# Kernel tuning notes

Hardware: AMD Instinct MI355X
Metric: run time of the kernel (lower is better)

The kernel has to match this reference:

```python
import jax, jax.numpy as jnp
import numpy as np

N = 65536          # particles
E = 524288         # relations (avg degree 8)
RIG = 4096         # rigid instance = particles [0, RIG); fluid = [RIG, N)
PSTEPS = 2
ATTR, STATE, RELD, NF = 3, 6, 1, 128
DT = 1.0 / 60.0
MEAN_P = np.zeros(3, np.float32); STD_P = np.ones(3, np.float32)
MEAN_V = np.zeros(3, np.float32); STD_V = np.ones(3, np.float32)


def _lin(x, w, b):
    return x @ w.T + b  # torch Linear convention: w is [out, in]


def setup_inputs() -> dict:
    key = jax.random.key(0)
    ks = iter(jax.random.split(key, 40))
    d = {}
    d["state"] = jax.random.normal(next(ks), (N, STATE), jnp.float32)
    d["attr"] = jax.random.normal(next(ks), (N, ATTR), jnp.float32)
    d["Ra"] = jax.random.normal(next(ks), (E, RELD), jnp.float32)
    d["rel_recv"] = jax.random.randint(next(ks), (E,), 0, N, jnp.int32)
    d["rel_send"] = jax.random.randint(next(ks), (E,), 0, N, jnp.int32)

    def w(shape):
        return jax.random.normal(next(ks), shape, jnp.float32) / np.sqrt(shape[1])

    d["pe_w0"] = w((NF, ATTR + 2 * STATE)); d["pe_b0"] = jnp.zeros(NF)
    d["pe_w1"] = w((NF, NF)); d["pe_b1"] = jnp.zeros(NF)
    d["re_w0"] = w((NF, 2 * ATTR + 4 * STATE + RELD)); d["re_b0"] = jnp.zeros(NF)
    d["re_w1"] = w((NF, NF)); d["re_b1"] = jnp.zeros(NF)
    d["re_w2"] = w((NF, NF)); d["re_b2"] = jnp.zeros(NF)
    d["rp_w"] = w((NF, 3 * NF)); d["rp_b"] = jnp.zeros(NF)
    d["pp_w"] = w((NF, 2 * NF)); d["pp_b"] = jnp.zeros(NF)
    d["rg_w0"] = w((NF, NF)); d["rg_b0"] = jnp.zeros(NF)
    d["rg_w1"] = w((NF, NF)); d["rg_b1"] = jnp.zeros(NF)
    d["rg_w2"] = w((7, NF)); d["rg_b2"] = jnp.zeros(7)
    d["fl_w0"] = w((NF, NF)); d["fl_b0"] = jnp.zeros(NF)
    d["fl_w1"] = w((NF, NF)); d["fl_b1"] = jnp.zeros(NF)
    d["fl_w2"] = w((3, NF)); d["fl_b2"] = jnp.zeros(3)
    return d


def reference(state, attr, Ra, rel_recv, rel_send,
              pe_w0, pe_b0, pe_w1, pe_b1,
              re_w0, re_b0, re_w1, re_b1, re_w2, re_b2,
              rp_w, rp_b, pp_w, pp_b,
              rg_w0, rg_b0, rg_w1, rg_b1, rg_w2, rg_b2,
              fl_w0, fl_b0, fl_w1, fl_b1, fl_w2, fl_b2):
    relu = jax.nn.relu
    mean_p = jnp.asarray(MEAN_P); std_p = jnp.asarray(STD_P)
    mean_v = jnp.asarray(MEAN_V); std_v = jnp.asarray(STD_V)

    # rigid-body offset (state minus instance centroid for the rigid instance)
    offset = jnp.zeros_like(state).at[:RIG].set(
        state[:RIG] - jnp.mean(state[:RIG], axis=0))
    attr2 = jnp.concatenate([attr, offset], axis=1)        # [N, ATTR+STATE]

    # f_O^enc: particle encoder on [attr2, state]
    pe_in = jnp.concatenate([attr2, state], axis=1)         # [N, 15]
    particle_encode = relu(_lin(relu(_lin(pe_in, pe_w0, pe_b0)), pe_w1, pe_b1))

    # f_R^enc: relation encoder on gathered receiver/sender features
    rel_in = jnp.concatenate([attr2[rel_recv], attr2[rel_send],
                              state[rel_recv], state[rel_send], Ra], axis=1)  # [E, 31]
    h = relu(_lin(rel_in, re_w0, re_b0))
    h = relu(_lin(h, re_w1, re_b1))
    relation_encode = relu(_lin(h, re_w2, re_b2))           # [E, NF]

    # propagation: gather effects -> f_R -> scatter-add -> f_O
    effect = jnp.zeros((N, NF), state.dtype)
    for _ in range(PSTEPS):
        r_eff = effect[rel_recv]                            # [E, NF]
        s_eff = effect[rel_send]                            # [E, NF]
        rel_eff = relu(_lin(jnp.concatenate(
            [relation_encode, r_eff, s_eff], axis=1), rp_w, rp_b))
        agg = jax.ops.segment_sum(rel_eff, rel_recv, num_segments=N)  # Rr @ rel_eff
        effect = relu(_lin(jnp.concatenate(
            [particle_encode, agg], axis=1), pp_w, pp_b))   # residual=False

    # rigid predictor: quaternion + translation of the rigid body
    pooled = jnp.mean(effect[:RIG], axis=0)                 # [NF]
    t = _lin(relu(_lin(relu(_lin(pooled, rg_w0, rg_b0)), rg_w1, rg_b1)), rg_w2, rg_b2)
    q = t[:4] / jnp.linalg.norm(t[:4])
    w, x, y, z = q[0], q[1], q[2], q[3]
    R = jnp.stack([
        jnp.stack([1.0 - 2 * (y * y + z * z), 2 * (x * y + z * w), 2 * (x * z - y * w)]),
        jnp.stack([2 * (x * y - z * w), 1.0 - 2 * (x * x + z * z), 2 * (y * z + x * w)]),
        jnp.stack([2 * (x * z + y * w), 2 * (y * z - x * w), 1.0 - 2 * (x * x + y * y)]),
    ])
    b = t[4:] * std_p
    p0 = state[:RIG, :3] * std_p + mean_p
    c = jnp.mean(p0, axis=0)
    p1 = (p0 - c) @ R + b + c
    v = (p1 - p0) / DT
    pred_rigid = (v - mean_v) / std_v                       # [RIG, 3]

    # fluid predictor: per-particle MLP
    f = relu(_lin(effect[RIG:], fl_w0, fl_b0))
    f = relu(_lin(f, fl_w1, fl_b1))
    pred_fluid = _lin(f, fl_w2, fl_b2)                      # [N-RIG, 3]

    return jnp.concatenate([pred_rigid, pred_fluid], axis=0)  # [N, 3]
```

## Files before the change

kernel.cpp:

```cpp
#include <hip/hip_runtime.h>
#include <hip/hip_bf16.h>
#include <cstdio>

#define N_P   65536
#define N_E   524288
#define RIG_  4096

typedef __attribute__((ext_vector_type(8))) short bf16x8;
typedef __attribute__((ext_vector_type(4))) float f32x4;
typedef unsigned short u16;
typedef unsigned int   u32;

__device__ __forceinline__ u16 f2b(float x) {
    __hip_bfloat16 h = __float2bfloat16(x);
    return *(u16*)&h;
}
__device__ __forceinline__ float b2f(u16 u) {
    union { unsigned u; float f; } c; c.u = ((unsigned)u) << 16; return c.f;
}
__device__ __forceinline__ unsigned pk2(float x, float y) {
    return (unsigned)f2b(x) | ((unsigned)f2b(y) << 16);
}
#define MFMA(a,b,c) __builtin_amdgcn_mfma_f32_16x16x32_bf16((a),(b),(c),0,0,0)

__global__ __launch_bounds__(256) void k_hist(const int* __restrict__ recv,
                                              u32* __restrict__ cnt) {
    int i = blockIdx.x * 256 + threadIdx.x;
    if (i < N_E) atomicAdd(&cnt[recv[i]], 1u);
}
__global__ __launch_bounds__(256) void k_scan1(u32* __restrict__ data,
                                               u32* __restrict__ bsum) {
    __shared__ u32 s[256];
    int t = threadIdx.x, g = blockIdx.x * 256 + t;
    u32 v = data[g];
    s[t] = v; __syncthreads();
    for (int o = 1; o < 256; o <<= 1) {
        u32 x = (t >= o) ? s[t - o] : 0u;
        __syncthreads(); s[t] += x; __syncthreads();
    }
    data[g] = s[t] - v;
    if (t == 255) bsum[blockIdx.x] = s[255];
}
__global__ __launch_bounds__(256) void k_scan2(u32* __restrict__ bsum) {
    __shared__ u32 s[256];
    int t = threadIdx.x;
    u32 v = bsum[t];
    s[t] = v; __syncthreads();
    for (int o = 1; o < 256; o <<= 1) {
        u32 x = (t >= o) ? s[t - o] : 0u;
        __syncthreads(); s[t] += x; __syncthreads();
    }
    bsum[t] = s[t] - v;
}
__global__ __launch_bounds__(256) void k_scan3(u32* __restrict__ data,
                                               const u32* __restrict__ bsum) {
    int g = blockIdx.x * 256 + threadIdx.x;
    data[g] += bsum[blockIdx.x];
}
__global__ __launch_bounds__(256) void k_scatter(const int* __restrict__ recv,
                                                 const int* __restrict__ send,
                                                 u32* __restrict__ head,
                                                 u32* __restrict__ perm,
                                                 int* __restrict__ srecv,
                                                 int* __restrict__ ssend) {
    int i = blockIdx.x * 256 + threadIdx.x;
    if (i < N_E) {
        int n = recv[i];
        u32 pos = atomicAdd(&head[n], 1u);
        perm[pos] = (u32)i;
        srecv[pos] = n;
        ssend[pos] = send[i];
    }
}

struct CvtJob { const float* src; u16* dst; int n; int mode; int bstart; };
struct CvtArgs { CvtJob j[14]; };

__global__ __launch_bounds__(256) void k_cvt_all(CvtArgs a) {
    int b = blockIdx.x;
    int ji = 0;
    #pragma unroll
    for (int k = 1; k < 14; k++) if (b >= a.j[k].bstart) ji = k;
    CvtJob jb = a.j[ji];
    int i = (b - jb.bstart) * 256 + threadIdx.x;
    if (i >= jb.n) return;
    if (jb.mode == 0) {
        jb.dst[i] = f2b(jb.src[i]);
    } else if (jb.mode == 2) {
        int r = i >> 7;
        jb.dst[i] = (r < 3) ? f2b(jb.src[i]) : 0;
    } else if (jb.mode == 3) {
        int r = i >> 7, c = i & 127;
        jb.dst[i] = f2b(jb.src[r * 384 + c]);
    } else if (jb.mode == 4) {
        int r = i >> 7, c = i & 127;
        jb.dst[i] = f2b(jb.src[r * 256 + c]);
    } else if (jb.mode == 5) {
        int r = i >> 5, c = i & 31;
        float v = 0.f;
        if (c < 9)       v = jb.src[r * 31 + c];
        else if (c < 15) v = jb.src[r * 31 + 18 + (c - 9)];
        jb.dst[i] = f2b(v);
    } else if (jb.mode == 6) {
        int r = i >> 5, c = i & 31;
        float v = 0.f;
        if (c < 9)       v = jb.src[r * 31 + 9 + c];
        else if (c < 15) v = jb.src[r * 31 + 24 + (c - 9)];
        jb.dst[i] = f2b(v);
    } else {
        int r = i >> 5, c = i & 31;
        jb.dst[i] = (c < 15) ? f2b(jb.src[r * 15 + c]) : 0;
    }
}

__global__ __launch_bounds__(256) void k_centroid(const float* __restrict__ state,
                                                  float* __restrict__ cent) {
    int d = blockIdx.x;
    __shared__ float red[256];
    float s = 0.f;
    for (int r = threadIdx.x; r < RIG_; r += 256) s += state[r * 6 + d];
    red[threadIdx.x] = s; __syncthreads();
    for (int o = 128; o > 0; o >>= 1) {
        if (threadIdx.x < o) red[threadIdx.x] += red[threadIdx.x + o];
        __syncthreads();
    }
    if (threadIdx.x == 0) cent[d] = red[0] / (float)RIG_;
}

__global__ __launch_bounds__(256) void k_particle_ext(
        const float* __restrict__ state, const float* __restrict__ attr,
        const float* __restrict__ cent,
        const u16* __restrict__ w0r, const u16* __restrict__ w0s,
        const u16* __restrict__ pew0, const float* __restrict__ pe_b0,
        const u16* __restrict__ pew1, const float* __restrict__ pe_b1,
        const u16* __restrict__ wp,
        u16* __restrict__ P, u16* __restrict__ Q, u16* __restrict__ T) {
    __shared__ float in_s[64][16];
    __shared__ u16 INF[64 * 32];
    __shared__ __align__(16) u16 BUF[64 * 128];
    __shared__ float b0_s[128], b1_s[128];
    int t = threadIdx.x;
    int base = blockIdx.x * 64;
    if (t < 128) { b0_s[t] = pe_b0[t]; b1_s[t] = pe_b1[t]; }
    for (int it = t; it < 64 * 15; it += 256) {
        int r = it / 15, c = it % 15;
        int p = base + r;
        float v;
        if (c < 3)      v = attr[p * 3 + c];
        else if (c < 9) v = (p < RIG_) ? (state[p * 6 + (c - 3)] - cent[c - 3]) : 0.0f;
        else            v = state[p * 6 + (c - 9)];
        in_s[r][c] = v;
    }
    __syncthreads();
    int wv = t >> 6, kq4 = (t >> 4) & 3, m = t & 15;
    {
        int e = wv * 16 + m;
        u16 tmp[8];
        #pragma unroll
        for (int j = 0; j < 8; j++) {
            int k = kq4 * 8 + j;
            tmp[j] = (k < 15) ? f2b(in_s[e][k]) : (u16)0;
        }
        *(uint4*)&INF[((wv * 4 + kq4) * 16 + m) * 8] = *(uint4*)tmp;
    }
    int lane = t & 63, mm = lane & 15, quad = lane >> 4;
    bf16x8 af0 = *(const bf16x8*)&INF[((wv * 4 + quad) * 16 + mm) * 8];
    {
        f32x4 acc[8] = {};
        #pragma unroll
        for (int nt = 0; nt < 8; nt++) {
            bf16x8 bf = *(const bf16x8*)(w0r + (size_t)(nt * 16 + mm) * 32 + quad * 8);
            acc[nt] = MFMA(af0, bf, acc[nt]);
        }
        #pragma unroll
        for (int nt = 0; nt < 8; nt++) {
            int col = nt * 16 + mm;
            #pragma unroll
            for (int rg = 0; rg < 4; rg++) {
                int row = wv * 16 + quad * 4 + rg;
                P[(size_t)(base + row) * 128 + col] = f2b(acc[nt][rg]);
            }
        }
    }
    {
        f32x4 acc[8] = {};
        #pragma unroll
        for (int nt = 0; nt < 8; nt++) {
            bf16x8 bf = *(const bf16x8*)(w0s + (size_t)(nt * 16 + mm) * 32 + quad * 8);
            acc[nt] = MFMA(af0, bf, acc[nt]);
        }
        #pragma unroll
        for (int nt = 0; nt < 8; nt++) {
            int col = nt * 16 + mm;
            #pragma unroll
            for (int rg = 0; rg < 4; rg++) {
                int row = wv * 16 + quad * 4 + rg;
                Q[(size_t)(base + row) * 128 + col] = f2b(acc[nt][rg]);
            }
        }
    }
    {
        f32x4 acc[8] = {};
        #pragma unroll
        for (int nt = 0; nt < 8; nt++) {
            bf16x8 bf = *(const bf16x8*)(pew0 + (size_t)(nt * 16 + mm) * 32 + quad * 8);
            acc[nt] = MFMA(af0, bf, acc[nt]);
        }
        #pragma unroll
        for (int nt = 0; nt < 8; nt++) {
            int col = nt * 16 + mm;
            #pragma unroll
            for (int rg = 0; rg < 4; rg++) {
                BUF[((wv * 16 + (col >> 3)) * 16 + quad * 4 + rg) * 8 + (col & 7)] =
                    f2b(fmaxf(acc[nt][rg] + b0_s[col], 0.f));
            }
        }
    }
    {
        f32x4 acc[8] = {};
        for (int kc = 0; kc < 4; kc++) {
            bf16x8 af = *(const bf16x8*)&BUF[((wv * 16 + kc * 4 + quad) * 16 + mm) * 8];
            #pragma unroll
            for (int nt = 0; nt < 8; nt++) {
                bf16x8 bf = *(const bf16x8*)(pew1 + (size_t)(nt * 16 + mm) * 128 + kc * 32 + quad * 8);
                acc[nt] = MFMA(af, bf, acc[nt]);
            }
        }
        #pragma unroll
        for (int nt = 0; nt < 8; nt++) {
            int col = nt * 16 + mm;
            #pragma unroll
            for (int rg = 0; rg < 4; rg++) {
                BUF[((wv * 16 + (col >> 3)) * 16 + quad * 4 + rg) * 8 + (col & 7)] =
                    f2b(fmaxf(acc[nt][rg] + b1_s[col], 0.f));
            }
        }
    }
    {
        f32x4 acc[8] = {};
        for (int kc = 0; kc < 4; kc++) {
            bf16x8 af = *(const bf16x8*)&BUF[((wv * 16 + kc * 4 + quad) * 16 + mm) * 8];
            #pragma unroll
            for (int nt = 0; nt < 8; nt++) {
                bf16x8 bf = *(const bf16x8*)(wp + (size_t)(nt * 16 + mm) * 128 + kc * 32 + quad * 8);
                acc[nt] = MFMA(af, bf, acc[nt]);
            }
        }
        #pragma unroll
        for (int nt = 0; nt < 8; nt++) {
            int col = nt * 16 + mm;
            #pragma unroll
            for (int rg = 0; rg < 4; rg++) {
                int row = wv * 16 + quad * 4 + rg;
                T[(size_t)(base + row) * 128 + col] = f2b(acc[nt][rg]);
            }
        }
    }
}

__global__ __launch_bounds__(512, 4) void k_rel(
        const u16* __restrict__ P, const u16* __restrict__ Q,
        const float* __restrict__ Ra, const u32* __restrict__ perm,
        const int* __restrict__ srecv, const int* __restrict__ ssend,
        const float* __restrict__ re_w0_raw, const float* __restrict__ b0,
        const u16* __restrict__ w1b, const float* __restrict__ b1,
        const u16* __restrict__ w2b, const float* __restrict__ b2,
        const u16* __restrict__ wreb, const float* __restrict__ rpb,
        u16* __restrict__ Z, float* __restrict__ agg) {
    __shared__ __align__(16) u16 BUFA[64 * 130];
    __shared__ __align__(16) u16 BUFB[64 * 130];
    __shared__ int rv_s[64];
    __shared__ float wRa_s[128], b0_s[128];
    int t = threadIdx.x;
    if (t < 128) { wRa_s[t] = re_w0_raw[t * 31 + 30]; b0_s[t] = b0[t]; }
    int w = t >> 6, lane = t & 63, mm = lane & 15, quad = lane >> 4;
    int colw = w * 16 + mm;
    bf16x8 W1f[4], W2f[4], WEf[4];
    #pragma unroll
    for (int kc = 0; kc < 4; kc++) {
        W1f[kc] = *(const bf16x8*)(w1b  + (size_t)colw * 128 + kc * 32 + quad * 8);
        W2f[kc] = *(const bf16x8*)(w2b  + (size_t)colw * 128 + kc * 32 + quad * 8);
        WEf[kc] = *(const bf16x8*)(wreb + (size_t)colw * 128 + kc * 32 + quad * 8);
    }
    float b1c = b1[colw], b2c = b2[colw], rpbc = rpb[colw];
    int es = t >> 3, cs2 = (t & 7) * 2;
    int egs = es >> 4, ms = es & 15;
    int sseg = t >> 7, cseg = t & 127;
    const long NT = N_E / 64;
    const long stride = gridDim.x;

    long tile = blockIdx.x;
    uint4 upC0, upC1, uqC0, uqC1; float raC; int rvC;
    {
        long nb = tile * 64;
        int rvp = srecv[nb + es], svp = ssend[nb + es];
        u32 pv = perm[nb + es];
        rvC = srecv[nb + (t & 63)];
        raC = Ra[pv];
        upC0 = *(const uint4*)(P + (size_t)rvp * 128 + (size_t)cs2 * 8);
        upC1 = *(const uint4*)(P + (size_t)rvp * 128 + (size_t)(cs2 + 1) * 8);
        uqC0 = *(const uint4*)(Q + (size_t)svp * 128 + (size_t)cs2 * 8);
        uqC1 = *(const uint4*)(Q + (size_t)svp * 128 + (size_t)(cs2 + 1) * 8);
    }
    for (; tile < NT; tile += stride) {
        long base = tile * 64;
        long ntile = tile + stride;
        bool hn = ntile < NT;
        __syncthreads();
        int rvpN = 0, svpN = 0, rvN = 0; u32 pvN = 0;
        if (hn) {
            long nb = ntile * 64;
            rvpN = srecv[nb + es]; svpN = ssend[nb + es];
            pvN  = perm[nb + es];  rvN  = srecv[nb + (t & 63)];
        }
        if (t < 64) rv_s[t] = rvC;
        {
            #pragma unroll
            for (int ci = 0; ci < 2; ci++) {
                int kq = cs2 + ci;
                uint4 up = ci ? upC1 : upC0;
                uint4 uq = ci ? uqC1 : uqC0;
                const u16* pp = (const u16*)&up; const u16* qq = (const u16*)&uq;
                u16 outv[8];
                #pragma unroll
                for (int j = 0; j < 8; j++) {
                    int c = kq * 8 + j;
                    float v = b2f(pp[j]) + b2f(qq[j]) + raC * wRa_s[c] + b0_s[c];
                    outv[j] = f2b(fmaxf(v, 0.f));
                }
                *(uint4*)&BUFA[((egs * 16 + kq) * 16 + ms) * 8] = *(uint4*)outv;
            }
        }
        __syncthreads();
        uint4 upN0{}, upN1{}, uqN0{}, uqN1{}; float raN = 0.f;
        if (hn) {
            raN  = Ra[pvN];
            upN0 = *(const uint4*)(P + (size_t)rvpN * 128 + (size_t)cs2 * 8);
            upN1 = *(const uint4*)(P + (size_t)rvpN * 128 + (size_t)(cs2 + 1) * 8);
            uqN0 = *(const uint4*)(Q + (size_t)svpN * 128 + (size_t)cs2 * 8);
            uqN1 = *(const uint4*)(Q + (size_t)svpN * 128 + (size_t)(cs2 + 1) * 8);
        }
        {
            f32x4 acc[4] = {};
            #pragma unroll
            for (int eg = 0; eg < 4; eg++)
                #pragma unroll
                for (int kc = 0; kc < 4; kc++) {
                    bf16x8 af = *(const bf16x8*)&BUFA[((eg * 16 + kc * 4 + quad) * 16 + mm) * 8];
                    acc[eg] = MFMA(af, W1f[kc], acc[eg]);
                }
            #pragma unroll
            for (int eg = 0; eg < 4; eg++)
                #pragma unroll
                for (int rg = 0; rg < 4; rg++)
                    BUFB[((eg * 16 + (colw >> 3)) * 16 + quad * 4 + rg) * 8 + (colw & 7)] =
                        f2b(fmaxf(acc[eg][rg] + b1c, 0.f));
        }
        __syncthreads();
        {
            f32x4 acc[4] = {};
            #pragma unroll
            for (int eg = 0; eg < 4; eg++)
                #pragma unroll
                for (int kc = 0; kc < 4; kc++) {
                    bf16x8 af = *(const bf16x8*)&BUFB[((eg * 16 + kc * 4 + quad) * 16 + mm) * 8];
                    acc[eg] = MFMA(af, W2f[kc], acc[eg]);
                }
            #pragma unroll
            for (int eg = 0; eg < 4; eg++)
                #pragma unroll
                for (int rg = 0; rg < 4; rg++)
                    BUFA[((eg * 16 + (colw >> 3)) * 16 + quad * 4 + rg) * 8 + (colw & 7)] =
                        f2b(fmaxf(acc[eg][rg] + b2c, 0.f));
        }
        __syncthreads();
        {
            f32x4 zacc[4] = {};
            #pragma unroll
            for (int eg = 0; eg < 4; eg++)
                #pragma unroll
                for (int kc = 0; kc < 4; kc++) {
                    bf16x8 af = *(const bf16x8*)&BUFA[((eg * 16 + kc * 4 + quad) * 16 + mm) * 8];
                    zacc[eg] = MFMA(af, WEf[kc], zacc[eg]);
                }
            #pragma unroll
            for (int eg = 0; eg < 4; eg++)
                #pragma unroll
                for (int rg = 0; rg < 4; rg++)
                    Z[(base + eg * 16 + quad * 4 + rg) * 128 + colw] = f2b(zacc[eg][rg]);
            #pragma unroll
            for (int eg = 0; eg < 4; eg++)
                #pragma unroll
                for (int rg = 0; rg < 4; rg++)
                    BUFB[(eg * 16 + quad * 4 + rg) * 130 + colw] =
                        f2b(fmaxf(zacc[eg][rg] + rpbc, 0.f));
        }
        __syncthreads();
        {
            int r0 = sseg * 16;
            int cur = rv_s[r0];
            float a = b2f(BUFB[r0 * 130 + cseg]);
            bool first = true;
            for (int rr = r0 + 1; rr < r0 + 16; rr++) {
                int n = rv_s[rr];
                float v = b2f(BUFB[rr * 130 + cseg]);
                if (n == cur) a += v;
                else {
                    if (first) atomicAdd(&agg[(size_t)cur * 128 + cseg], a);
                    else       agg[(size_t)cur * 128 + cseg] = a;
                    first = false; cur = n; a = v;
                }
            }
            atomicAdd(&agg[(size_t)cur * 128 + cseg], a);
        }
        if (hn) { upC0 = upN0; upC1 = upN1; uqC0 = uqN0; uqC1 = uqN1; raC = raN; rvC = rvN; }
    }
}

__global__ __launch_bounds__(256) void k_node2(
        const float* __restrict__ agg, const u16* __restrict__ T,
        const u16* __restrict__ wab, const float* __restrict__ ppb,
        u16* __restrict__ effb,
        const u16* __restrict__ wrb, const u16* __restrict__ wsb,
        u16* __restrict__ U, u16* __restrict__ V) {
    __shared__ __align__(16) u16 AF[64 * 128];
    int t = threadIdx.x;
    long base = (long)blockIdx.x * 64;
    int wv = t >> 6, kq4 = (t >> 4) & 3, m = t & 15;
    {
        long node = base + wv * 16 + m;
        #pragma unroll
        for (int i = 0; i < 4; i++) {
            int kq = kq4 + 4 * i;
            const float* src = agg + node * 128 + kq * 8;
            float4 f0 = *(const float4*)src, f1 = *(const float4*)(src + 4);
            uint4 v;
            v.x = pk2(f0.x, f0.y); v.y = pk2(f0.z, f0.w);
            v.z = pk2(f1.x, f1.y); v.w = pk2(f1.z, f1.w);
            *(uint4*)&AF[((wv * 16 + kq) * 16 + m) * 8] = v;
        }
    }
    int lane = t & 63, mm = lane & 15, quad = lane >> 4;
    f32x4 acc[8] = {};
    for (int kc = 0; kc < 4; kc++) {
        bf16x8 af = *(const bf16x8*)&AF[((wv * 16 + kc * 4 + quad) * 16 + mm) * 8];
        #pragma unroll
        for (int nt = 0; nt < 8; nt++) {
            bf16x8 bf = *(const bf16x8*)(wab + (size_t)(nt * 16 + mm) * 128 + kc * 32 + quad * 8);
            acc[nt] = MFMA(af, bf, acc[nt]);
        }
    }
    #pragma unroll
    for (int nt = 0; nt < 8; nt++) {
        int col = nt * 16 + mm;
        #pragma unroll
        for (int rg = 0; rg < 4; rg++) {
            long row = base + wv * 16 + quad * 4 + rg;
            float v = acc[nt][rg] + b2f(T[row * 128 + col]) + ppb[col];
            u16 e = f2b(fmaxf(v, 0.f));
            if (effb) effb[row * 128 + col] = e;
            AF[((wv * 16 + (col >> 3)) * 16 + quad * 4 + rg) * 8 + (col & 7)] = e;
        }
    }
    {
        f32x4 au[8] = {};
        for (int kc = 0; kc < 4; kc++) {
            bf16x8 af = *(const bf16x8*)&AF[((wv * 16 + kc * 4 + quad) * 16 + mm) * 8];
            #pragma unroll
            for (int nt = 0; nt < 8; nt++) {
                bf16x8 bu = *(const bf16x8*)(wrb + (size_t)(nt * 16 + mm) * 128 + kc * 32 + quad * 8);
                au[nt] = MFMA(af, bu, au[nt]);
            }
        }
        #pragma unroll
        for (int nt = 0; nt < 8; nt++) {
            int col = nt * 16 + mm;
            #pragma unroll
            for (int rg = 0; rg < 4; rg++) {
                long row = base + wv * 16 + quad * 4 + rg;
                U[row * 128 + col] = f2b(au[nt][rg]);
            }
        }
    }
    {
        f32x4 av[8] = {};
        for (int kc = 0; kc < 4; kc++) {
            bf16x8 af = *(const bf16x8*)&AF[((wv * 16 + kc * 4 + quad) * 16 + mm) * 8];
            #pragma unroll
            for (int nt = 0; nt < 8; nt++) {
                bf16x8 bv = *(const bf16x8*)(wsb + (size_t)(nt * 16 + mm) * 128 + kc * 32 + quad * 8);
                av[nt] = MFMA(af, bv, av[nt]);
            }
        }
        #pragma unroll
        for (int nt = 0; nt < 8; nt++) {
            int col = nt * 16 + mm;
            #pragma unroll
            for (int rg = 0; rg < 4; rg++) {
                long row = base + wv * 16 + quad * 4 + rg;
                V[row * 128 + col] = f2b(av[nt][rg]);
            }
        }
    }
}

#define HPAD 136
__global__ __launch_bounds__(256) void k_node2fl(
        const float* __restrict__ agg, const u16* __restrict__ T,
        const u16* __restrict__ wab, const float* __restrict__ ppb,
        u16* __restrict__ effb,
        const u16* __restrict__ w0b, const float* __restrict__ b0,
        const u16* __restrict__ w1b, const float* __restrict__ b1,
        const u16* __restrict__ w2b, const float* __restrict__ b2,
        float* __restrict__ out) {
    __shared__ __align__(16) u16 H[64 * HPAD];
    int t = threadIdx.x;
    long base = (long)blockIdx.x * 64;
    bool fluid = (base >= RIG_);
    int wv = t >> 6, kq4 = (t >> 4) & 3, m = t & 15;
    {
        long node = base + wv * 16 + m;
        #pragma unroll
        for (int i = 0; i < 4; i++) {
            int kq = kq4 + 4 * i;
            const float* src = agg + node * 128 + kq * 8;
            float4 f0 = *(const float4*)src, f1 = *(const float4*)(src + 4);
            uint4 v;
            v.x = pk2(f0.x, f0.y); v.y = pk2(f0.z, f0.w);
            v.z = pk2(f1.x, f1.y); v.w = pk2(f1.z, f1.w);
            *(uint4*)&H[((wv * 16 + kq) * 16 + m) * 8] = v;
        }
    }
    int lane = t & 63, mm = lane & 15, quad = lane >> 4;
    f32x4 acc[8] = {};
    for (int kc = 0; kc < 4; kc++) {
        bf16x8 af = *(const bf16x8*)&H[((wv * 16 + kc * 4 + quad) * 16 + mm) * 8];
        #pragma unroll
        for (int nt = 0; nt < 8; nt++) {
            bf16x8 bf = *(const bf16x8*)(wab + (size_t)(nt * 16 + mm) * 128 + kc * 32 + quad * 8);
            acc[nt] = MFMA(af, bf, acc[nt]);
        }
    }
    if (!fluid) {
        #pragma unroll
        for (int nt = 0; nt < 8; nt++) {
            int col = nt * 16 + mm;
            #pragma unroll
            for (int rg = 0; rg < 4; rg++) {
                long row = base + wv * 16 + quad * 4 + rg;
                float v = acc[nt][rg] + b2f(T[row * 128 + col]) + ppb[col];
                effb[row * 128 + col] = f2b(fmaxf(v, 0.f));
            }
        }
        return;
    }
    __syncthreads();
    #pragma unroll
    for (int nt = 0; nt < 8; nt++) {
        int col = nt * 16 + mm;
        #pragma unroll
        for (int rg = 0; rg < 4; rg++) {
            long row = base + wv * 16 + quad * 4 + rg;
            float v = acc[nt][rg] + b2f(T[row * 128 + col]) + ppb[col];
            H[(wv * 16 + quad * 4 + rg) * HPAD + col] = f2b(fmaxf(v, 0.f));
        }
    }
    {
        f32x4 a8[8] = {};
        for (int kc = 0; kc < 4; kc++) {
            bf16x8 af = *(const bf16x8*)&H[(wv * 16 + mm) * HPAD + kc * 32 + quad * 8];
            #pragma unroll
            for (int nt = 0; nt < 8; nt++) {
                bf16x8 bf = *(const bf16x8*)(w0b + (size_t)(nt * 16 + mm) * 128 + kc * 32 + quad * 8);
                a8[nt] = MFMA(af, bf, a8[nt]);
            }
        }
        #pragma unroll
        for (int nt = 0; nt < 8; nt++) {
            int col = nt * 16 + mm;
            float bv = b0[col];
            #pragma unroll
            for (int rg = 0; rg < 4; rg++) {
                int row = wv * 16 + quad * 4 + rg;
                H[row * HPAD + col] = f2b(fmaxf(a8[nt][rg] + bv, 0.f));
            }
        }
    }
    {
        f32x4 a8[8] = {};
        for (int kc = 0; kc < 4; kc++) {
            bf16x8 af = *(const bf16x8*)&H[(wv * 16 + mm) * HPAD + kc * 32 + quad * 8];
            #pragma unroll
            for (int nt = 0; nt < 8; nt++) {
                bf16x8 bf = *(const bf16x8*)(w1b + (size_t)(nt * 16 + mm) * 128 + kc * 32 + quad * 8);
                a8[nt] = MFMA(af, bf, a8[nt]);
            }
        }
        #pragma unroll
        for (int nt = 0; nt < 8; nt++) {
            int col = nt * 16 + mm;
            float bv = b1[col];
            #pragma unroll
            for (int rg = 0; rg < 4; rg++) {
                int row = wv * 16 + quad * 4 + rg;
                H[row * HPAD + col] = f2b(fmaxf(a8[nt][rg] + bv, 0.f));
            }
        }
    }
    {
        f32x4 a1 = {};
        for (int kc = 0; kc < 4; kc++) {
            bf16x8 af = *(const bf16x8*)&H[(wv * 16 + mm) * HPAD + kc * 32 + quad * 8];
            bf16x8 bf = *(const bf16x8*)(w2b + (size_t)mm * 128 + kc * 32 + quad * 8);
            a1 = MFMA(af, bf, a1);
        }
        if (mm < 3) {
            float bv = b2[mm];
            #pragma unroll
            for (int rg = 0; rg < 4; rg++) {
                long row = base + wv * 16 + quad * 4 + rg;
                out[row * 3 + mm] = a1[rg] + bv;
            }
        }
    }
}

__global__ __launch_bounds__(256) void k_edge2(
        const u16* __restrict__ Z, const u16* __restrict__ U, const u16* __restrict__ V,
        const int* __restrict__ srecv, const int* __restrict__ ssend,
        const float* __restrict__ rpb, float* __restrict__ agg) {
    __shared__ __align__(16) u16 S16[64 * 136];
    __shared__ int rv_s[64];
    __shared__ float rpb_s[128];
    int t = threadIdx.x;
    long base = (long)blockIdx.x * 64;
    if (t < 64) rv_s[t] = srecv[base + t];
    if (t < 128) rpb_s[t] = rpb[t];
    int r = t >> 2, q = t & 3;
    int rv = srecv[base + r];
    int sv = ssend[base + r];
    long zb = (base + r) * 128;
    size_t ub = (size_t)rv * 128, vb = (size_t)sv * 128;
    __syncthreads();
    #pragma unroll
    for (int i = 0; i < 4; i++) {
        int c0 = q * 32 + i * 8;
        uint4 uz = *(const uint4*)(Z + zb + c0);
        uint4 uu = *(const uint4*)(U + ub + c0);
        uint4 uv = *(const uint4*)(V + vb + c0);
        const u16* zz = (const u16*)&uz; const u16* pu = (const u16*)&uu; const u16* pv = (const u16*)&uv;
        u16 o[8];
        #pragma unroll
        for (int j = 0; j < 8; j++)
            o[j] = f2b(fmaxf(b2f(zz[j]) + b2f(pu[j]) + b2f(pv[j]) + rpb_s[c0 + j], 0.f));
        *(uint4*)&S16[r * 136 + c0] = *(uint4*)o;
    }
    __syncthreads();
    {
        int s = t >> 7, col = t & 127;
        int r0 = s * 32;
        int cur = rv_s[r0];
        float a = b2f(S16[r0 * 136 + col]);
        bool first = true;
        for (int rr = r0 + 1; rr < r0 + 32; rr++) {
            int n = rv_s[rr];
            float v = b2f(S16[rr * 136 + col]);
            if (n == cur) a += v;
            else {
                if (first) atomicAdd(&agg[(size_t)cur * 128 + col], a);
                else       agg[(size_t)cur * 128 + col] = a;
                first = false; cur = n; a = v;
            }
        }
        atomicAdd(&agg[(size_t)cur * 128 + col], a);
    }
}

__global__ __launch_bounds__(256) void k_pool(const u16* __restrict__ effb,
                                              float* __restrict__ pooled) {
    int f = blockIdx.x;
    __shared__ float red[256];
    float s = 0.f;
    for (int r = threadIdx.x; r < RIG_; r += 256) s += b2f(effb[(size_t)r * 128 + f]);
    red[threadIdx.x] = s; __syncthreads();
    for (int o = 128; o > 0; o >>= 1) {
        if (threadIdx.x < o) red[threadIdx.x] += red[threadIdx.x + o];
        __syncthreads();
    }
    if (threadIdx.x == 0) pooled[f] = red[0] / (float)RIG_;
}

__global__ __launch_bounds__(128) void k_rigid_head(
        const float* __restrict__ pooled,
        const float* __restrict__ w0, const float* __restrict__ b0,
        const float* __restrict__ w1, const float* __restrict__ b1,
        const float* __restrict__ w2, const float* __restrict__ b2,
        float* __restrict__ rig) {
    __shared__ float pl[128], ha[128], hb[128], tv[7];
    int t = threadIdx.x;
    pl[t] = pooled[t];
    __syncthreads();
    float a = b0[t];
    for (int k = 0; k < 128; k++) a += w0[t * 128 + k] * pl[k];
    ha[t] = fmaxf(a, 0.f);
    __syncthreads();
    a = b1[t];
    for (int k = 0; k < 128; k++) a += w1[t * 128 + k] * ha[k];
    hb[t] = fmaxf(a, 0.f);
    __syncthreads();
    if (t < 7) {
        float s = b2[t];
        for (int k = 0; k < 128; k++) s += w2[t * 128 + k] * hb[k];
        tv[t] = s;
    }
    __syncthreads();
    if (t == 0) {
        float w = tv[0], x = tv[1], y = tv[2], z = tv[3];
        float n = sqrtf(w * w + x * x + y * y + z * z);
        w /= n; x /= n; y /= n; z /= n;
        rig[0] = 1.f - 2.f * (y * y + z * z); rig[1] = 2.f * (x * y + z * w); rig[2] = 2.f * (x * z - y * w);
        rig[3] = 2.f * (x * y - z * w); rig[4] = 1.f - 2.f * (x * x + z * z); rig[5] = 2.f * (y * z + x * w);
        rig[6] = 2.f * (x * z + y * w); rig[7] = 2.f * (y * z - x * w); rig[8] = 1.f - 2.f * (x * x + y * y);
        rig[9] = tv[4]; rig[10] = tv[5]; rig[11] = tv[6];
    }
}

__global__ __launch_bounds__(256) void k_rigid_out(
        const float* __restrict__ state, const float* __restrict__ cent,
        const float* __restrict__ rig, float* __restrict__ out) {
    int i = blockIdx.x * 256 + threadIdx.x;
    if (i >= RIG_) return;
    float p0[3], d[3];
    #pragma unroll
    for (int k = 0; k < 3; k++) { p0[k] = state[i * 6 + k]; d[k] = p0[k] - cent[k]; }
    #pragma unroll
    for (int j = 0; j < 3; j++) {
        float p1 = rig[0 * 3 + j] * d[0] + rig[1 * 3 + j] * d[1] + rig[2 * 3 + j] * d[2]
                 + rig[9 + j] + cent[j];
        out[i * 3 + j] = (p1 - p0[j]) * 60.0f;
    }
}

extern "C" void kernel_launch(void* const* d_in, const int* in_sizes, int n_in,
                              void* d_out, int out_size, void* d_ws, size_t ws_size,
                              hipStream_t stream) {
    const float* state = (const float*)d_in[0];
    const float* attr  = (const float*)d_in[1];
    const float* Ra    = (const float*)d_in[2];
    const int*   recv  = (const int*)d_in[3];
    const int*   send  = (const int*)d_in[4];
    const float* pe_w0 = (const float*)d_in[5];  const float* pe_b0 = (const float*)d_in[6];
    const float* pe_w1 = (const float*)d_in[7];  const float* pe_b1 = (const float*)d_in[8];
    const float* re_w0 = (const float*)d_in[9];  const float* re_b0 = (const float*)d_in[10];
    const float* re_w1 = (const float*)d_in[11]; const float* re_b1 = (const float*)d_in[12];
    const float* re_w2 = (const float*)d_in[13]; const float* re_b2 = (const float*)d_in[14];
    const float* rp_w  = (const float*)d_in[15]; const float* rp_b  = (const float*)d_in[16];
    const float* pp_w  = (const float*)d_in[17]; const float* pp_b  = (const float*)d_in[18];
    const float* rg_w0 = (const float*)d_in[19]; const float* rg_b0 = (const float*)d_in[20];
    const float* rg_w1 = (const float*)d_in[21]; const float* rg_b1 = (const float*)d_in[22];
    const float* rg_w2 = (const float*)d_in[23]; const float* rg_b2 = (const float*)d_in[24];
    const float* fl_w0 = (const float*)d_in[25]; const float* fl_b0 = (const float*)d_in[26];
    const float* fl_w1 = (const float*)d_in[27]; const float* fl_b1 = (const float*)d_in[28];
    const float* fl_w2 = (const float*)d_in[29]; const float* fl_b2 = (const float*)d_in[30];
    float* out = (float*)d_out;

    char* p = (char*)d_ws;
    auto alloc = [&](size_t bytes) { char* r = p; p += (bytes + 255) / 256 * 256; return r; };
    float* cent    = (float*)alloc(8 * 4);
    float* pooled  = (float*)alloc(128 * 4);
    float* rig     = (float*)alloc(16 * 4);
    u32*   rowhead = (u32*)alloc((size_t)N_P * 4);
    u32*   bsum    = (u32*)alloc(256 * 4);
    u32*   perm    = (u32*)alloc((size_t)N_E * 4);
    int*   srecv   = (int*)alloc((size_t)N_E * 4);
    int*   ssend   = (int*)alloc((size_t)N_E * 4);
    float* agg     = (float*)alloc((size_t)N_P * 128 * 4);
    u16*   Z       = (u16*)alloc((size_t)N_E * 128 * 2);
    u16*   effb    = (u16*)alloc((size_t)N_P * 128 * 2);
    u16*   T       = (u16*)alloc((size_t)N_P * 128 * 2);
    u16*   P       = (u16*)alloc((size_t)N_P * 128 * 2);
    u16*   Q       = (u16*)alloc((size_t)N_P * 128 * 2);
    u16*   wreb    = (u16*)alloc(128 * 128 * 2);
    u16*   wrb     = (u16*)alloc(128 * 128 * 2);
    u16*   wsb     = (u16*)alloc(128 * 128 * 2);
    u16*   wpb     = (u16*)alloc(128 * 128 * 2);
    u16*   wab     = (u16*)alloc(128 * 128 * 2);
    u16*   rw1b    = (u16*)alloc(128 * 128 * 2);
    u16*   rw2b    = (u16*)alloc(128 * 128 * 2);
    u16*   pew1b   = (u16*)alloc(128 * 128 * 2);
    u16*   flw0b   = (u16*)alloc(128 * 128 * 2);
    u16*   flw1b   = (u16*)alloc(128 * 128 * 2);
    u16*   flw2b   = (u16*)alloc(16 * 128 * 2);
    u16*   w0rb    = (u16*)alloc(128 * 32 * 2);
    u16*   w0sb    = (u16*)alloc(128 * 32 * 2);
    u16*   pew0b   = (u16*)alloc(128 * 32 * 2);
    size_t need = (size_t)(p - (char*)d_ws);
    if (ws_size < need) {
        fprintf(stderr, "kernel_launch: ws_size %zu < needed %zu\n", ws_size, need);
        return;
    }
    u16* U = P; u16* V = Q;

    hipMemsetAsync(rowhead, 0, (size_t)N_P * 4, stream);
    k_hist<<<N_E / 256, 256, 0, stream>>>(recv, rowhead);
    k_scan1<<<N_P / 256, 256, 0, stream>>>(rowhead, bsum);
    k_scan2<<<1, 256, 0, stream>>>(bsum);
    k_scan3<<<N_P / 256, 256, 0, stream>>>(rowhead, bsum);
    k_scatter<<<N_E / 256, 256, 0, stream>>>(recv, send, rowhead, perm, srecv, ssend);

    CvtArgs ca;
    int bs = 0;
    auto addjob = [&](int idx, const float* s, u16* d, int n, int mode) {
        ca.j[idx] = {s, d, n, mode, bs};
        bs += (n + 255) / 256;
    };
    addjob(0,  rp_w,        wreb,  128 * 128, 3);
    addjob(1,  rp_w + 128,  wrb,   128 * 128, 3);
    addjob(2,  rp_w + 256,  wsb,   128 * 128, 3);
    addjob(3,  pp_w,        wpb,   128 * 128, 4);
    addjob(4,  pp_w + 128,  wab,   128 * 128, 4);
    addjob(5,  re_w1,       rw1b,  128 * 128, 0);
    addjob(6,  re_w2,       rw2b,  128 * 128, 0);
    addjob(7,  pe_w1,       pew1b, 128 * 128, 0);
    addjob(8,  fl_w0,       flw0b, 128 * 128, 0);
    addjob(9,  fl_w1,       flw1b, 128 * 128, 0);
    addjob(10, fl_w2,       flw2b, 16 * 128,  2);
    addjob(11, re_w0,       w0rb,  128 * 32,  5);
    addjob(12, re_w0,       w0sb,  128 * 32,  6);
    addjob(13, pe_w0,       pew0b, 128 * 32,  7);
    k_cvt_all<<<bs, 256, 0, stream>>>(ca);

    k_centroid<<<6, 256, 0, stream>>>(state, cent);
    k_particle_ext<<<N_P / 64, 256, 0, stream>>>(state, attr, cent,
                                                 w0rb, w0sb, pew0b, pe_b0,
                                                 pew1b, pe_b1, wpb, P, Q, T);

    hipMemsetAsync(agg, 0, (size_t)N_P * 128 * 4, stream);
    k_rel<<<512, 512, 0, stream>>>(P, Q, Ra, perm, srecv, ssend,
                                   re_w0, re_b0, rw1b, re_b1, rw2b, re_b2,
                                   wreb, rp_b, Z, agg);
    k_node2<<<N_P / 64, 256, 0, stream>>>(agg, T, wab, pp_b, nullptr, wrb, wsb, U, V);

    hipMemsetAsync(agg, 0, (size_t)N_P * 128 * 4, stream);
    k_edge2<<<N_E / 64, 256, 0, stream>>>(Z, U, V, srecv, ssend, rp_b, agg);
    k_node2fl<<<N_P / 64, 256, 0, stream>>>(agg, T, wab, pp_b, effb,
                                            flw0b, fl_b0, flw1b, fl_b1,
                                            flw2b, fl_b2, out);

    k_pool<<<128, 256, 0, stream>>>(effb, pooled);
    k_rigid_head<<<1, 128, 0, stream>>>(pooled, rg_w0, rg_b0, rg_w1, rg_b1, rg_w2, rg_b2, rig);
    k_rigid_out<<<(RIG_ + 255) / 256, 256, 0, stream>>>(state, cent, rig, out);
}
```

Before: 568.2 us.

## Stage Z through LDS for coalesced stores and use LDS-only barriers

The Z output of the relation MLP is now written to shared memory first and then copied to global memory with 16-byte coalesced stores, replacing scattered 2-byte stores. The bias+ReLU for the aggregation is moved into the segmented reduction. A custom barrier waits only on LDS counters, so pending global loads and stores are not drained at each sync. The top-of-loop barrier is removed by double-buffering the receiver index array. The risk is subtle ordering bugs if any global-memory dependency relied on the full barrier. LDS row padding also changes from 130 to 136.

Measured after the change: 562.5 us. Within noise of the previous version (-1.0%).

```diff
diff --git a/kernel.cpp b/kernel.cpp
--- a/kernel.cpp
+++ b/kernel.cpp
@@ -22,6 +22,10 @@
     return (unsigned)f2b(x) | ((unsigned)f2b(y) << 16);
 }
 #define MFMA(a,b,c) __builtin_amdgcn_mfma_f32_16x16x32_bf16((a),(b),(c),0,0,0)
+
+__device__ __forceinline__ void bar_l() {
+    asm volatile("s_waitcnt lgkmcnt(0)\n\ts_barrier" ::: "memory");
+}
 
 __global__ __launch_bounds__(256) void k_hist(const int* __restrict__ recv,
                                               u32* __restrict__ cnt) {
@@ -267,12 +271,15 @@
         const u16* __restrict__ w2b, const float* __restrict__ b2,
         const u16* __restrict__ wreb, const float* __restrict__ rpb,
         u16* __restrict__ Z, float* __restrict__ agg) {
-    __shared__ __align__(16) u16 BUFA[64 * 130];
-    __shared__ __align__(16) u16 BUFB[64 * 130];
-    __shared__ int rv_s[64];
-    __shared__ float wRa_s[128], b0_s[128];
+    __shared__ __align__(16) u16 BUFA[64 * 136];
+    __shared__ __align__(16) u16 BUFB[64 * 136];
+    __shared__ int rv_s[2][64];
+    __shared__ float wRa_s[128], b0_s[128], rpb_s[128];
     int t = threadIdx.x;
-    if (t < 128) { wRa_s[t] = re_w0_raw[t * 31 + 30]; b0_s[t] = b0[t]; }
+    if (t < 128) {
+        wRa_s[t] = re_w0_raw[t * 31 + 30];
+        b0_s[t] = b0[t]; rpb_s[t] = rpb[t];
+    }
     int w = t >> 6, lane = t & 63, mm = lane & 15, quad = lane >> 4;
     int colw = w * 16 + mm;
     bf16x8 W1f[4], W2f[4], WEf[4];
@@ -282,10 +289,11 @@
         W2f[kc] = *(const bf16x8*)(w2b  + (size_t)colw * 128 + kc * 32 + quad * 8);
         WEf[kc] = *(const bf16x8*)(wreb + (size_t)colw * 128 + kc * 32 + quad * 8);
     }
-    float b1c = b1[colw], b2c = b2[colw], rpbc = rpb[colw];
+    float b1c = b1[colw], b2c = b2[colw];
     int es = t >> 3, cs2 = (t & 7) * 2;
     int egs = es >> 4, ms = es & 15;
     int sseg = t >> 7, cseg = t & 127;
+    int zrow = t >> 3, zc0 = (t & 7) * 16;
     const long NT = N_E / 64;
     const long stride = gridDim.x;
 
@@ -302,18 +310,19 @@
         uqC0 = *(const uint4*)(Q + (size_t)svp * 128 + (size_t)cs2 * 8);
         uqC1 = *(const uint4*)(Q + (size_t)svp * 128 + (size_t)(cs2 + 1) * 8);
     }
+    __syncthreads();
+    int p = 0;
     for (; tile < NT; tile += stride) {
         long base = tile * 64;
         long ntile = tile + stride;
         bool hn = ntile < NT;
-        __syncthreads();
         int rvpN = 0, svpN = 0, rvN = 0; u32 pvN = 0;
         if (hn) {
             long nb = ntile * 64;
             rvpN = srecv[nb + es]; svpN = ssend[nb + es];
             pvN  = perm[nb + es];  rvN  = srecv[nb + (t & 63)];
         }
-        if (t < 64) rv_s[t] = rvC;
+        if (t < 64) rv_s[p][t] = rvC;
         {
             #pragma unroll
             for (int ci = 0; ci < 2; ci++) {
@@ -331,7 +340,7 @@
                 *(uint4*)&BUFA[((egs * 16 + kq) * 16 + ms) * 8] = *(uint4*)outv;
             }
         }
-        __syncthreads();
+        bar_l();
         uint4 upN0{}, upN1{}, uqN0{}, uqN1{}; float raN = 0.f;
         if (hn) {
             raN  = Ra[pvN];
@@ -356,7 +365,7 @@
                     BUFB[((eg * 16 + (colw >> 3)) * 16 + quad * 4 + rg) * 8 + (colw & 7)] =
                         f2b(fmaxf(acc[eg][rg] + b1c, 0.f));
         }
-        __syncthreads();
+        bar_l();
         {
             f32x4 acc[4] = {};
             #pragma unroll
@@ -373,7 +382,7 @@
                     BUFA[((eg * 16 + (colw >> 3)) * 16 + quad * 4 + rg) * 8 + (colw & 7)] =
                         f2b(fmaxf(acc[eg][rg] + b2c, 0.f));
         }
-        __syncthreads();
+        bar_l();
         {
             f32x4 zacc[4] = {};
             #pragma unroll
@@ -387,23 +396,23 @@
             for (int eg = 0; eg < 4; eg++)
                 #pragma unroll
                 for (int rg = 0; rg < 4; rg++)
-                    Z[(base + eg * 16 + quad * 4 + rg) * 128 + colw] = f2b(zacc[eg][rg]);
-            #pragma unroll
-            for (int eg = 0; eg < 4; eg++)
-                #pragma unroll
-                for (int rg = 0; rg < 4; rg++)
-                    BUFB[(eg * 16 + quad * 4 + rg) * 130 + colw] =
-                        f2b(fmaxf(zacc[eg][rg] + rpbc, 0.f));
-        }
-        __syncthreads();
+                    BUFB[(eg * 16 + quad * 4 + rg) * 136 + colw] = f2b(zacc[eg][rg]);
+        }
+        bar_l();
+        {
+            uint4 z0 = *(const uint4*)&BUFB[zrow * 136 + zc0];
+            uint4 z1 = *(const uint4*)&BUFB[zrow * 136 + zc0 + 8];
+            *(uint4*)&Z[(base + zrow) * 128 + zc0]     = z0;
+            *(uint4*)&Z[(base + zrow) * 128 + zc0 + 8] = z1;
+        }
         {
             int r0 = sseg * 16;
-            int cur = rv_s[r0];
-            float a = b2f(BUFB[r0 * 130 + cseg]);
+            int cur = rv_s[p][r0];
+            float a = fmaxf(b2f(BUFB[r0 * 136 + cseg]) + rpb_s[cseg], 0.f);
             bool first = true;
             for (int rr = r0 + 1; rr < r0 + 16; rr++) {
-                int n = rv_s[rr];
-                float v = b2f(BUFB[rr * 130 + cseg]);
+                int n = rv_s[p][rr];
+                float v = fmaxf(b2f(BUFB[rr * 136 + cseg]) + rpb_s[cseg], 0.f);
                 if (n == cur) a += v;
                 else {
                     if (first) atomicAdd(&agg[(size_t)cur * 128 + cseg], a);
@@ -414,6 +423,7 @@
             atomicAdd(&agg[(size_t)cur * 128 + cseg], a);
         }
         if (hn) { upC0 = upN0; upC1 = upN1; uqC0 = uqN0; uqC1 = uqN1; raC = raN; rvC = rvN; }
+        p ^= 1;
     }
 }
 
@@ -641,7 +651,7 @@
     int sv = ssend[base + r];
     long zb = (base + r) * 128;
     size_t ub = (size_t)rv * 128, vb = (size_t)sv * 128;
-    __syncthreads();
+    bar_l();
     #pragma unroll
     for (int i = 0; i < 4; i++) {
         int c0 = q * 32 + i * 8;
@@ -655,7 +665,7 @@
             o[j] = f2b(fmaxf(b2f(zz[j]) + b2f(pu[j]) + b2f(pv[j]) + rpb_s[c0 + j], 0.f));
         *(uint4*)&S16[r * 136 + c0] = *(uint4*)o;
     }
-    __syncthreads();
+    bar_l();
     {
         int s = t >> 7, col = t & 127;
         int r0 = s * 32;
```
